# Performance work log

Measured on AMD Instinct MI355X. Metric: run time of the kernel, lower is better.

The kernel has to match this reference:

```python
import jax, jax.numpy as jnp
import numpy as np
from jax import lax

B, C, H, W = 8, 256, 64, 64
A = 9                      # anchors per location (3 scales x 3 ratios)
STRIDE = 16
IMG = 1024                 # image_size
POST_NMS = 1000            # post_nms_top_n (also used as pre-NMS slice, as in source)
NMS_THR = 0.7
BBOX_XFORM_CLIP = 4.135166556742356  # log(1000/16)


def make_anchors():
    # ordering must match torch reshape (B,4,-1): index = a*H*W + h*W + w
    scales = jnp.array([128.0, 256.0, 512.0], dtype=jnp.float32)
    ratios = jnp.array([0.5, 1.0, 2.0], dtype=jnp.float32)
    ws = (scales[:, None] / jnp.sqrt(ratios)[None, :]).reshape(-1)  # [A]
    hs = (scales[:, None] * jnp.sqrt(ratios)[None, :]).reshape(-1)  # [A]
    cx = (jnp.arange(W, dtype=jnp.float32) + 0.5) * STRIDE
    cy = (jnp.arange(H, dtype=jnp.float32) + 0.5) * STRIDE
    cx = jnp.broadcast_to(cx[None, None, :], (A, H, W))
    cy = jnp.broadcast_to(cy[None, :, None], (A, H, W))
    aw = jnp.broadcast_to(ws[:, None, None], (A, H, W))
    ah = jnp.broadcast_to(hs[:, None, None], (A, H, W))
    anchors = jnp.stack([cx - aw / 2, cy - ah / 2, cx + aw / 2, cy + ah / 2], axis=-1)
    return anchors.reshape(-1, 4)  # [K,4] xyxy


def conv2d(x, w, b, pad):
    y = lax.conv_general_dilated(x, w, (1, 1), [(pad, pad), (pad, pad)],
                                 dimension_numbers=("NCHW", "OIHW", "NCHW"))
    return y + b[None, :, None, None]


def decode(t, anchors):
    # t: [K,4] (tx,ty,tw,th); anchors: [K,4] xyxy -> boxes xyxy
    aw = anchors[:, 2] - anchors[:, 0]
    ah = anchors[:, 3] - anchors[:, 1]
    acx = anchors[:, 0] + 0.5 * aw
    acy = anchors[:, 1] + 0.5 * ah
    cx = t[:, 0] * aw + acx
    cy = t[:, 1] * ah + acy
    w = jnp.exp(jnp.clip(t[:, 2], -BBOX_XFORM_CLIP, BBOX_XFORM_CLIP)) * aw
    h = jnp.exp(jnp.clip(t[:, 3], -BBOX_XFORM_CLIP, BBOX_XFORM_CLIP)) * ah
    return jnp.stack([cx - 0.5 * w, cy - 0.5 * h, cx + 0.5 * w, cy + 0.5 * h], axis=-1)


def box_iou(a, b):
    area_a = (a[:, 2] - a[:, 0]) * (a[:, 3] - a[:, 1])
    area_b = (b[:, 2] - b[:, 0]) * (b[:, 3] - b[:, 1])
    lt = jnp.maximum(a[:, None, :2], b[None, :, :2])
    rb = jnp.minimum(a[:, None, 2:], b[None, :, 2:])
    wh = jnp.clip(rb - lt, 0.0)
    inter = wh[..., 0] * wh[..., 1]
    return inter / (area_a[:, None] + area_b[None, :] - inter)


def filter_one(boxes, scores):
    # boxes [K,4], scores [K]. Faithful to source: torch.sort ascending,
    # slice to POST_NMS, then class-agnostic greedy NMS, pad to POST_NMS.
    order = jnp.argsort(lax.stop_gradient(scores))        # ascending (torch.sort default)
    idx = order[:POST_NMS]
    b = boxes[idx]
    s = scores[idx]
    # batched_nms internally processes boxes in descending-score order
    o2 = jnp.argsort(-lax.stop_gradient(s))
    b2 = b[o2]
    s2 = s[o2]
    iou = box_iou(b2, b2)  # [POST_NMS, POST_NMS]
    N = POST_NMS
    pos = jnp.arange(N)

    def body(i, keep):
        sup = (iou[i] > NMS_THR) & (pos > i) & keep[i]
        return keep & ~sup

    keep = lax.fori_loop(0, N, body, jnp.ones((N,), dtype=bool))
    # pack kept boxes (descending-score order) to the front, zero-pad the rest
    perm = jnp.argsort(jnp.where(keep, pos, N + pos))
    valid = pos < jnp.sum(keep)
    out_b = jnp.where(valid[:, None], b2[perm], 0.0)
    out_s = jnp.where(valid, s2[perm], 0.0)
    return out_b, out_s


def setup_inputs() -> dict:
    key = jax.random.key(0)
    ks = jax.random.split(key, 5)
    x = jax.random.normal(ks[0], (B, C, H, W), dtype=jnp.float32)
    conv_w = jax.random.normal(ks[1], (C, C, 3, 3), dtype=jnp.float32) * 0.01
    conv_b = jnp.zeros((C,), dtype=jnp.float32)
    box_w = jax.random.normal(ks[2], (4 * A, C, 1, 1), dtype=jnp.float32) * 0.01
    box_b = jnp.zeros((4 * A,), dtype=jnp.float32)
    obj_w = jax.random.normal(ks[3], (A, C, 1, 1), dtype=jnp.float32) * 0.01
    obj_b = jnp.zeros((A,), dtype=jnp.float32)
    return {"x": x, "conv_w": conv_w, "conv_b": conv_b,
            "box_w": box_w, "box_b": box_b, "obj_w": obj_w, "obj_b": obj_b}


def reference(x, conv_w, conv_b, box_w, box_b, obj_w, obj_b):
    feats = jax.nn.relu(conv2d(x, conv_w, conv_b, 1))        # [B,C,H,W]
    t = conv2d(feats, box_w, box_b, 0)                        # [B,4A,H,W]
    o = conv2d(feats, obj_w, obj_b, 0)                        # [B,A,H,W]
    t = t.reshape(B, 4, -1).transpose(0, 2, 1)                # [B,K,4]
    obj = o.reshape(B, -1)                                    # [B,K]
    anchors = make_anchors()                                  # [K,4]
    props = jax.vmap(lambda ti: decode(ti, anchors))(t)       # [B,K,4]
    props = jnp.clip(props, 0.0, float(IMG))                  # clip_boxes_to_image
    out_b, out_s = jax.vmap(filter_one)(props, obj)           # [B,POST_NMS,4],[B,POST_NMS]
    return jnp.concatenate([out_b, out_s[..., None]], axis=-1)  # [B,POST_NMS,5]
```

## Files before the change

### kernel.cpp

```cpp
#include <hip/hip_runtime.h>

#define B_ 8
#define C_ 256
#define H_ 64
#define W_ 64
#define HW_ 4096
#define HP_ 66
#define HWP_ 4224
#define A_ 9
#define SITES 36864
#define NPOST 1000
#define XCLIPF 4.1351666f
#define IMGF 1024.0f

__device__ inline unsigned keyf(float v) {
  unsigned u = __float_as_uint(v);
  return (u & 0x80000000u) ? ~u : (u | 0x80000000u);
}

__device__ __forceinline__ float dpp_shr1(float v) {
  return __int_as_float(__builtin_amdgcn_update_dpp(
      0, __float_as_int(v), 0x111 , 0xf, 0xf, true));
}
__device__ __forceinline__ float dpp_shl1(float v) {
  return __int_as_float(__builtin_amdgcn_update_dpp(
      0, __float_as_int(v), 0x101 , 0xf, 0xf, true));
}

__global__ __launch_bounds__(256) void pad_x(
    const float* __restrict__ x, float* __restrict__ xp) {
  int t = blockIdx.x * 256 + threadIdx.x;
  int c4 = t & 15;
  int rr = (t >> 4) % HP_;
  int bc = t / (HP_ * 16);
  float4 v = make_float4(0.f, 0.f, 0.f, 0.f);
  if (rr >= 1 && rr <= 64)
    v = ((const float4*)x)[(size_t)bc * (HW_ / 4) + (size_t)(rr - 1) * 16 + c4];
  ((float4*)xp)[(size_t)bc * (HWP_ / 4) + (size_t)rr * 16 + c4] = v;
}

__global__ __launch_bounds__(256, 2) void conv3_4co(
    const float* __restrict__ xp, const float* __restrict__ w,
    const float* __restrict__ bias, float* __restrict__ feats) {
#pragma clang fp contract(off)
  int b       = blockIdx.x & 7;
  int j       = blockIdx.x >> 3;
  int quad    = j & 63;
  int quarter = j >> 6;
  int co0 = quad << 2;
  int row16 = threadIdx.x >> 4;
  int chunk = threadIdx.x & 15;
  int gr = (quarter << 4) + row16;
  int c0 = chunk << 2;

  const float* px0 = xp + (size_t)b * C_ * HWP_ + (size_t)gr * W_ + c0;
  const float* wp0 = w + (size_t)(co0 + 0) * (C_ * 9);
  const float* wp1 = w + (size_t)(co0 + 1) * (C_ * 9);
  const float* wp2 = w + (size_t)(co0 + 2) * (C_ * 9);
  const float* wp3 = w + (size_t)(co0 + 3) * (C_ * 9);

  float acc[4][4][9];
#pragma unroll
  for (int q = 0; q < 4; ++q)
#pragma unroll
    for (int p = 0; p < 4; ++p)
#pragma unroll
      for (int t = 0; t < 9; ++t) acc[q][p][t] = 0.f;

#pragma unroll 2
  for (int ci = 0; ci < C_; ++ci) {
    const float* pr = px0 + (size_t)ci * HWP_;
    float4 tA = ((const float4*)(pr      ))[0];
    float4 mA = ((const float4*)(pr +  64))[0];
    float4 bA = ((const float4*)(pr + 128))[0];

    float T[6], M[6], Bo[6];
    T[1]=tA.x;  T[2]=tA.y;  T[3]=tA.z;  T[4]=tA.w;
    M[1]=mA.x;  M[2]=mA.y;  M[3]=mA.z;  M[4]=mA.w;
    Bo[1]=bA.x; Bo[2]=bA.y; Bo[3]=bA.z; Bo[4]=bA.w;

    T[0]  = dpp_shr1(T[4]);   T[5]  = dpp_shl1(T[1]);
    M[0]  = dpp_shr1(M[4]);   M[5]  = dpp_shl1(M[1]);
    Bo[0] = dpp_shr1(Bo[4]);  Bo[5] = dpp_shl1(Bo[1]);

    float w9[4][9];
#pragma unroll
    for (int t = 0; t < 9; ++t) w9[0][t] = wp0[ci * 9 + t];
#pragma unroll
    for (int t = 0; t < 9; ++t) w9[1][t] = wp1[ci * 9 + t];
#pragma unroll
    for (int t = 0; t < 9; ++t) w9[2][t] = wp2[ci * 9 + t];
#pragma unroll
    for (int t = 0; t < 9; ++t) w9[3][t] = wp3[ci * 9 + t];

#pragma unroll
    for (int q = 0; q < 4; ++q)
#pragma unroll
      for (int p = 0; p < 4; ++p) {
        acc[q][p][0] = fmaf(w9[q][0], T[p],     acc[q][p][0]);
        acc[q][p][1] = fmaf(w9[q][1], T[p+1],   acc[q][p][1]);
        acc[q][p][2] = fmaf(w9[q][2], T[p+2],   acc[q][p][2]);
        acc[q][p][3] = fmaf(w9[q][3], M[p],     acc[q][p][3]);
        acc[q][p][4] = fmaf(w9[q][4], M[p+1],   acc[q][p][4]);
        acc[q][p][5] = fmaf(w9[q][5], M[p+2],   acc[q][p][5]);
        acc[q][p][6] = fmaf(w9[q][6], Bo[p],    acc[q][p][6]);
        acc[q][p][7] = fmaf(w9[q][7], Bo[p+1],  acc[q][p][7]);
        acc[q][p][8] = fmaf(w9[q][8], Bo[p+2],  acc[q][p][8]);
      }
  }

#pragma unroll
  for (int q = 0; q < 4; ++q) {
    float bv = bias[co0 + q];
    float ov[4];
#pragma unroll
    for (int p = 0; p < 4; ++p) {
      float a = 0.f;
#pragma unroll
      for (int t = 0; t < 9; ++t) a = a + acc[q][p][t];
      a = a + bv;
      ov[p] = a > 0.f ? a : 0.f;
    }
    float4* fo = (float4*)(feats + ((size_t)b * C_ + co0 + q) * HW_ + (size_t)gr * W_ + c0);
    fo[0] = make_float4(ov[0], ov[1], ov[2], ov[3]);
  }
}

__global__ __launch_bounds__(256) void conv1_split3(
    const float* __restrict__ feats,
    const float* __restrict__ box_w, const float* __restrict__ box_b,
    const float* __restrict__ obj_w, const float* __restrict__ obj_b,
    float* __restrict__ tbox, float* __restrict__ scores) {
#pragma clang fp contract(off)
  int gidx = blockIdx.x * 256 + threadIdx.x;
  int cgrp = gidx >> 15;
  int rem  = gidx & 32767;
  int b  = rem >> 12;
  int hw = rem & 4095;
  int cbase = cgrp * 15;
  const float* f = feats + (size_t)b * C_ * HW_ + hw;
  const float* wrow[15];
#pragma unroll
  for (int jj = 0; jj < 15; ++jj) {
    int c = cbase + jj;
    wrow[jj] = (c < 36) ? (box_w + (size_t)c * C_) : (obj_w + (size_t)(c - 36) * C_);
  }
  float acc[15];
#pragma unroll
  for (int jj = 0; jj < 15; ++jj) acc[jj] = 0.f;
  for (int ci = 0; ci < C_; ++ci) {
    float fv = f[(size_t)ci * HW_];
#pragma unroll
    for (int jj = 0; jj < 15; ++jj)
      acc[jj] = fmaf(wrow[jj][ci], fv, acc[jj]);
  }
#pragma unroll
  for (int jj = 0; jj < 15; ++jj) {
    int c = cbase + jj;
    if (c < 36) {
      int k = c / 9, a = c - k * 9;
      tbox[(size_t)b * 4 * SITES + (size_t)k * SITES + (size_t)a * HW_ + hw] = acc[jj] + box_b[c];
    } else {
      int a = c - 36;
      scores[(size_t)b * SITES + (size_t)a * HW_ + hw] = acc[jj] + obj_b[a];
    }
  }
}

__global__ __launch_bounds__(1024) void radix_select(
    const float* __restrict__ scores, unsigned* __restrict__ Kout,
    int* __restrict__ needEq, int* __restrict__ cnt, int* __restrict__ eqCnt) {
  int b = blockIdx.x;
  const float* s = scores + (size_t)b * SITES;
  __shared__ unsigned hist[256];
  __shared__ unsigned sh_prefix, sh_mask, sh_cless;
  __shared__ int sh_target;
  if (threadIdx.x == 0) { sh_prefix = 0; sh_mask = 0; sh_target = NPOST - 1; sh_cless = 0; }
  for (int shift = 24; shift >= 0; shift -= 8) {
    if (threadIdx.x < 256) hist[threadIdx.x] = 0;
    __syncthreads();
    unsigned prefix = sh_prefix, mask = sh_mask;
    for (int i = threadIdx.x; i < SITES; i += 1024) {
      unsigned k = keyf(s[i]);
      if ((k & mask) == prefix) atomicAdd(&hist[(k >> shift) & 255u], 1u);
    }
    __syncthreads();
    if (threadIdx.x == 0) {
      unsigned cum = 0; int t = sh_target; int v = 0;
      for (; v < 256; ++v) {
        unsigned h = hist[v];
        if (cum + h > (unsigned)t) break;
        cum += h;
      }
      sh_prefix |= ((unsigned)v) << shift;
      sh_mask   |= 0xFFu << shift;
      sh_target  = t - (int)cum;
      sh_cless  += cum;
    }
    __syncthreads();
  }
  if (threadIdx.x == 0) {
    Kout[b] = sh_prefix;
    needEq[b] = NPOST - (int)sh_cless;
    cnt[b] = 0;
    eqCnt[b] = 0;
  }
}

__global__ __launch_bounds__(256) void compact_sel(
    const float* __restrict__ scores, const unsigned* __restrict__ Kout,
    int* __restrict__ cnt, int* __restrict__ sel,
    int* __restrict__ eqCnt, int* __restrict__ eqList) {
  int b = blockIdx.x / 144;
  int i = (blockIdx.x % 144) * 256 + threadIdx.x;
  unsigned K = Kout[b];
  unsigned k = keyf(scores[(size_t)b * SITES + i]);
  if (k < K) {
    int pos = atomicAdd(&cnt[b], 1);
    sel[b * 1024 + pos] = i;
  } else if (k == K) {
    int e = atomicAdd(&eqCnt[b], 1);
    if (e < 4096) eqList[b * 4096 + e] = i;
  }
}

__global__ __launch_bounds__(256) void fix_eq(
    const int* __restrict__ cnt, const int* __restrict__ needEq,
    const int* __restrict__ eqCnt, const int* __restrict__ eqList,
    int* __restrict__ sel) {
  int b = blockIdx.x;
  int E = eqCnt[b]; if (E > 4096) E = 4096;
  int need = needEq[b];
  int base = cnt[b];
  const int* el = eqList + b * 4096;
  for (int t = threadIdx.x; t < E; t += 256) {
    int site = el[t];
    int rank = 0;
    for (int q = 0; q < E; ++q) rank += (el[q] < site);
    if (rank < need) sel[b * 1024 + base + rank] = site;
  }
}

__global__ __launch_bounds__(128) void order_decode(
    const float* __restrict__ scores, const int* __restrict__ sel,
    const float* __restrict__ tbox, float* __restrict__ s2, float* __restrict__ b2) {
#pragma clang fp contract(off)
  int b   = blockIdx.x >> 3;
  int r   = ((blockIdx.x & 7) * 125) + threadIdx.x;
  __shared__ float ss[NPOST];
  __shared__ int st[NPOST];
  for (int t = threadIdx.x; t < NPOST; t += 128) {
    int site = sel[b * 1024 + t];
    st[t] = site;
    ss[t] = scores[(size_t)b * SITES + site];
  }
  __syncthreads();
  if (threadIdx.x < 125) {
    float sr = ss[r]; int sir = st[r];
    int d = 0;
    for (int q = 0; q < NPOST; ++q) {
      float sq = ss[q];
      d += (int)((sq > sr) || (sq == sr && st[q] < sir));
    }
    s2[(size_t)b * NPOST + d] = sr;
    int site = sir;
    int a = site / HW_;
    int hw = site - a * HW_;
    int h = hw / W_, wc = hw - h * W_;
    int sidx = a / 3, ridx = a - sidx * 3;
    float scale = (sidx == 0) ? 128.f : ((sidx == 1) ? 256.f : 512.f);
    float ratio = (ridx == 0) ? 0.5f : ((ridx == 1) ? 1.0f : 2.0f);
    float sq = sqrtf(ratio);
    float wsa = scale / sq;
    float hsa = scale * sq;
    float cx = ((float)wc + 0.5f) * 16.f;
    float cy = ((float)h + 0.5f) * 16.f;
    float ax1 = cx - wsa * 0.5f;
    float ay1 = cy - hsa * 0.5f;
    float ax2 = cx + wsa * 0.5f;
    float ay2 = cy + hsa * 0.5f;
    float aw = ax2 - ax1, ah = ay2 - ay1;
    float m1 = 0.5f * aw, m2 = 0.5f * ah;
    float acx = ax1 + m1, acy = ay1 + m2;
    const float* tb = tbox + (size_t)b * 4 * SITES + site;
    float t0 = tb[0];
    float t1 = tb[SITES];
    float t2 = tb[2 * (size_t)SITES];
    float t3 = tb[3 * (size_t)SITES];
    if (t2 < -XCLIPF) t2 = -XCLIPF;
    if (t2 > XCLIPF) t2 = XCLIPF;
    if (t3 < -XCLIPF) t3 = -XCLIPF;
    if (t3 > XCLIPF) t3 = XCLIPF;
    float pm0 = t0 * aw;  float pcx = pm0 + acx;
    float pm1 = t1 * ah;  float pcy = pm1 + acy;
    float pw = expf(t2) * aw;
    float ph = expf(t3) * ah;
    float hw0 = 0.5f * pw, hh0 = 0.5f * ph;
    float x1 = pcx - hw0, y1 = pcy - hh0;
    float x2 = pcx + hw0, y2 = pcy + hh0;
    x1 = x1 < 0.f ? 0.f : (x1 > IMGF ? IMGF : x1);
    y1 = y1 < 0.f ? 0.f : (y1 > IMGF ? IMGF : y1);
    x2 = x2 < 0.f ? 0.f : (x2 > IMGF ? IMGF : x2);
    y2 = y2 < 0.f ? 0.f : (y2 > IMGF ? IMGF : y2);
    float* o = b2 + ((size_t)b * NPOST + d) * 4;
    o[0] = x1; o[1] = y1; o[2] = x2; o[3] = y2;
  }
}

__global__ __launch_bounds__(256) void mask_kernel(
    const float* __restrict__ b2, unsigned long long* __restrict__ sup) {
#pragma clang fp contract(off)
  int b = blockIdx.x / 63;
  int i0 = (blockIdx.x % 63) * 16;
  __shared__ float bs[NPOST * 4];
  __shared__ float area[NPOST];
  for (int t = threadIdx.x; t < NPOST * 4; t += 256) bs[t] = b2[(size_t)b * NPOST * 4 + t];
  __syncthreads();
  for (int t = threadIdx.x; t < NPOST; t += 256)
    area[t] = (bs[t * 4 + 2] - bs[t * 4]) * (bs[t * 4 + 3] - bs[t * 4 + 1]);
  __syncthreads();
  int i = i0 + (threadIdx.x & 15);
  int wd = threadIdx.x >> 4;
  if (i >= NPOST) return;
  float ax1 = bs[i * 4], ay1 = bs[i * 4 + 1], ax2 = bs[i * 4 + 2], ay2 = bs[i * 4 + 3];
  float aa = area[i];
  unsigned long long m = 0;
  for (int bit = 0; bit < 64; ++bit) {
    int j = wd * 64 + bit;
    if (j > i && j < NPOST) {
      float lx = fmaxf(ax1, bs[j * 4]);
      float ly = fmaxf(ay1, bs[j * 4 + 1]);
      float rx = fminf(ax2, bs[j * 4 + 2]);
      float ry = fminf(ay2, bs[j * 4 + 3]);
      float iw = rx - lx; if (iw < 0.f) iw = 0.f;
      float ih = ry - ly; if (ih < 0.f) ih = 0.f;
      float inter = iw * ih;
      float denom = (aa + area[j]) - inter;
      float iou = inter / denom;
      if (iou > 0.7f) m |= 1ull << bit;
    }
  }
  sup[((size_t)b * NPOST + i) * 16 + wd] = m;
}

__global__ __launch_bounds__(64) void nms_out(
    const unsigned long long* __restrict__ sup, const float* __restrict__ b2,
    const float* __restrict__ s2, float* __restrict__ out) {
  int b = blockIdx.x;
  int lane = threadIdx.x;
  unsigned long long kw = 0;
  if (lane < 16) kw = (lane < 15) ? ~0ull : ((1ull << 40) - 1);
  const unsigned long long* ms = sup + (size_t)b * NPOST * 16;
  unsigned long long mb[8];
#pragma unroll
  for (int k = 0; k < 8; ++k)
    mb[k] = (lane < 16) ? ms[(size_t)k * 16 + lane] : 0ull;
  for (int i0 = 0; i0 < NPOST; i0 += 8) {
    unsigned long long nb[8];
#pragma unroll
    for (int k = 0; k < 8; ++k) {
      int nx = i0 + 8 + k;
      nb[k] = (nx < NPOST && lane < 16) ? ms[(size_t)nx * 16 + lane] : 0ull;
    }
#pragma unroll
    for (int k = 0; k < 8; ++k) {
      int i = i0 + k;
      unsigned long long w = __shfl(kw, i >> 6, 64);
      if ((w >> (i & 63)) & 1ull) {
        if (lane < 16) kw &= ~mb[k];
      }
    }
#pragma unroll
    for (int k = 0; k < 8; ++k) mb[k] = nb[k];
  }
  __shared__ unsigned long long keeps[16];
  if (lane < 16) keeps[lane] = kw;
  __syncthreads();
  int total = 0;
#pragma unroll
  for (int k = 0; k < 16; ++k) total += __popcll(keeps[k]);
  for (int i = lane; i < NPOST; i += 64) {
    int w = i >> 6;
    int before = 0;
    for (int k = 0; k < w; ++k) before += __popcll(keeps[k]);
    before += __popcll(keeps[w] & ((1ull << (i & 63)) - 1));
    bool kept = (keeps[w] >> (i & 63)) & 1ull;
    if (kept) {
      size_t ob = (size_t)b * (NPOST * 5) + (size_t)before * 5;
      const float* src = b2 + ((size_t)b * NPOST + i) * 4;
      out[ob + 0] = src[0];
      out[ob + 1] = src[1];
      out[ob + 2] = src[2];
      out[ob + 3] = src[3];
      out[ob + 4] = s2[(size_t)b * NPOST + i];
    }
    if (i >= total) {
      size_t ob = (size_t)b * (NPOST * 5) + (size_t)i * 5;
      for (int c = 0; c < 5; ++c) out[ob + c] = 0.f;
    }
  }
}

extern "C" void kernel_launch(void* const* d_in, const int* in_sizes, int n_in,
                              void* d_out, int out_size, void* d_ws, size_t ws_size,
                              hipStream_t stream) {
  const float *x = nullptr, *conv_w = nullptr, *conv_b = nullptr,
              *box_w = nullptr, *box_b = nullptr, *obj_w = nullptr, *obj_b = nullptr;
  for (int i = 0; i < n_in; ++i) {
    switch (in_sizes[i]) {
      case 8388608: x = (const float*)d_in[i]; break;
      case 589824:  conv_w = (const float*)d_in[i]; break;
      case 256:     conv_b = (const float*)d_in[i]; break;
      case 9216:    box_w = (const float*)d_in[i]; break;
      case 36:      box_b = (const float*)d_in[i]; break;
      case 2304:    obj_w = (const float*)d_in[i]; break;
      case 9:       obj_b = (const float*)d_in[i]; break;
    }
  }
  float* out = (float*)d_out;

  char* p = (char*)d_ws;
  auto alloc = [&](size_t n) { char* q = p; p += (n + 255) & ~255ull; return (void*)q; };
  float* feats  = (float*)alloc((size_t)B_ * C_ * HW_ * 4);
  float* tbox   = (float*)alloc((size_t)B_ * 4 * SITES * 4);
  float* scores = (float*)alloc((size_t)B_ * SITES * 4);
  float* xpad   = (float*)alloc((size_t)B_ * C_ * HWP_ * 4);
  unsigned* Kout = (unsigned*)alloc(B_ * 4);
  int* needEq    = (int*)alloc(B_ * 4);
  int* cnt       = (int*)alloc(B_ * 4);
  int* eqCnt     = (int*)alloc(B_ * 4);
  int* eqList    = (int*)alloc((size_t)B_ * 4096 * 4);
  int* sel       = (int*)alloc((size_t)B_ * 1024 * 4);
  float* s2      = (float*)alloc((size_t)B_ * NPOST * 4);
  float* b2      = (float*)alloc((size_t)B_ * NPOST * 4 * 4);
  unsigned long long* sup = (unsigned long long*)alloc((size_t)B_ * NPOST * 16 * 8);

  hipLaunchKernelGGL(pad_x, dim3(B_ * C_ * HP_ * 16 / 256), dim3(256), 0, stream, x, xpad);
  hipLaunchKernelGGL(conv3_4co, dim3(B_ * 64 * 4), dim3(256), 0, stream,
                     xpad, conv_w, conv_b, feats);
  hipLaunchKernelGGL(conv1_split3, dim3(3 * B_ * HW_ / 256), dim3(256), 0, stream,
                     feats, box_w, box_b, obj_w, obj_b, tbox, scores);
  hipLaunchKernelGGL(radix_select, dim3(B_), dim3(1024), 0, stream,
                     scores, Kout, needEq, cnt, eqCnt);
  hipLaunchKernelGGL(compact_sel, dim3(B_ * 144), dim3(256), 0, stream,
                     scores, Kout, cnt, sel, eqCnt, eqList);
  hipLaunchKernelGGL(fix_eq, dim3(B_), dim3(256), 0, stream,
                     cnt, needEq, eqCnt, eqList, sel);
  hipLaunchKernelGGL(order_decode, dim3(B_ * 8), dim3(128), 0, stream,
                     scores, sel, tbox, s2, b2);
  hipLaunchKernelGGL(mask_kernel, dim3(B_ * 63), dim3(256), 0, stream, b2, sup);
  hipLaunchKernelGGL(nms_out, dim3(B_), dim3(64), 0, stream, sup, b2, s2, out);
}
```

Before: 1.020 ms.

## Fuse top-k select, compaction, tie fix and sort-decode into one kernel; pack conv weights

Merges radix_select, compact_sel, fix_eq and order_decode into a single per-batch 1024-thread kernel that keeps the selection lists in shared memory, removing three launches and global round-trips. It also adds a pack_w kernel that reorders conv weights so the four output channels' 36 weights per input channel are contiguous, for more uniform scalar loads in the 3x3 conv. The fused kernel runs only 8 blocks and does the compaction serially per block instead of over 1152 blocks, which lowers parallelism. Weight packing runs on every call, adding a small kernel.

Result: faster. 978.9 us (-4.0%).

```diff
diff --git a/kernel.cpp b/kernel.cpp
--- a/kernel.cpp
+++ b/kernel.cpp
@@ -39,8 +39,19 @@
   ((float4*)xp)[(size_t)bc * (HWP_ / 4) + (size_t)rr * 16 + c4] = v;
 }
 
+__global__ __launch_bounds__(256) void pack_w(
+    const float* __restrict__ w, float* __restrict__ wq) {
+  int idx = blockIdx.x * 256 + threadIdx.x;
+  int quad = idx / (256 * 36);
+  int rem  = idx % (256 * 36);
+  int ci = rem / 36;
+  int k  = rem % 36;
+  int q = k / 9, t = k % 9;
+  wq[idx] = w[((size_t)(quad * 4 + q)) * (C_ * 9) + (size_t)ci * 9 + t];
+}
+
 __global__ __launch_bounds__(256, 2) void conv3_4co(
-    const float* __restrict__ xp, const float* __restrict__ w,
+    const float* __restrict__ xp, const float* __restrict__ wq,
     const float* __restrict__ bias, float* __restrict__ feats) {
 #pragma clang fp contract(off)
   int b       = blockIdx.x & 7;
@@ -54,10 +65,7 @@
   int c0 = chunk << 2;
 
   const float* px0 = xp + (size_t)b * C_ * HWP_ + (size_t)gr * W_ + c0;
-  const float* wp0 = w + (size_t)(co0 + 0) * (C_ * 9);
-  const float* wp1 = w + (size_t)(co0 + 1) * (C_ * 9);
-  const float* wp2 = w + (size_t)(co0 + 2) * (C_ * 9);
-  const float* wp3 = w + (size_t)(co0 + 3) * (C_ * 9);
+  const float* wqb = wq + (size_t)quad * (C_ * 36);
 
   float acc[4][4][9];
 #pragma unroll
@@ -83,15 +91,12 @@
     M[0]  = dpp_shr1(M[4]);   M[5]  = dpp_shl1(M[1]);
     Bo[0] = dpp_shr1(Bo[4]);  Bo[5] = dpp_shl1(Bo[1]);
 
+    const float* wrow = wqb + ci * 36;
     float w9[4][9];
 #pragma unroll
-    for (int t = 0; t < 9; ++t) w9[0][t] = wp0[ci * 9 + t];
-#pragma unroll
-    for (int t = 0; t < 9; ++t) w9[1][t] = wp1[ci * 9 + t];
-#pragma unroll
-    for (int t = 0; t < 9; ++t) w9[2][t] = wp2[ci * 9 + t];
-#pragma unroll
-    for (int t = 0; t < 9; ++t) w9[3][t] = wp3[ci * 9 + t];
+    for (int q = 0; q < 4; ++q)
+#pragma unroll
+      for (int t = 0; t < 9; ++t) w9[q][t] = wrow[q * 9 + t];
 
 #pragma unroll
     for (int q = 0; q < 4; ++q)
@@ -167,15 +172,24 @@
   }
 }
 
-__global__ __launch_bounds__(1024) void radix_select(
-    const float* __restrict__ scores, unsigned* __restrict__ Kout,
-    int* __restrict__ needEq, int* __restrict__ cnt, int* __restrict__ eqCnt) {
+__global__ __launch_bounds__(1024) void select_sort_decode(
+    const float* __restrict__ scores, const float* __restrict__ tbox,
+    float* __restrict__ s2, float* __restrict__ b2) {
+#pragma clang fp contract(off)
   int b = blockIdx.x;
   const float* s = scores + (size_t)b * SITES;
   __shared__ unsigned hist[256];
   __shared__ unsigned sh_prefix, sh_mask, sh_cless;
   __shared__ int sh_target;
-  if (threadIdx.x == 0) { sh_prefix = 0; sh_mask = 0; sh_target = NPOST - 1; sh_cless = 0; }
+  __shared__ int sh_cnt, sh_eq;
+  __shared__ int sh_sel[1024];
+  __shared__ int sh_eqList[4096];
+  __shared__ float ss[NPOST];
+  __shared__ int st[NPOST];
+  if (threadIdx.x == 0) {
+    sh_prefix = 0; sh_mask = 0; sh_target = NPOST - 1; sh_cless = 0;
+    sh_cnt = 0; sh_eq = 0;
+  }
   for (int shift = 24; shift >= 0; shift -= 8) {
     if (threadIdx.x < 256) hist[threadIdx.x] = 0;
     __syncthreads();
@@ -199,63 +213,38 @@
     }
     __syncthreads();
   }
-  if (threadIdx.x == 0) {
-    Kout[b] = sh_prefix;
-    needEq[b] = NPOST - (int)sh_cless;
-    cnt[b] = 0;
-    eqCnt[b] = 0;
-  }
-}
-
-__global__ __launch_bounds__(256) void compact_sel(
-    const float* __restrict__ scores, const unsigned* __restrict__ Kout,
-    int* __restrict__ cnt, int* __restrict__ sel,
-    int* __restrict__ eqCnt, int* __restrict__ eqList) {
-  int b = blockIdx.x / 144;
-  int i = (blockIdx.x % 144) * 256 + threadIdx.x;
-  unsigned K = Kout[b];
-  unsigned k = keyf(scores[(size_t)b * SITES + i]);
-  if (k < K) {
-    int pos = atomicAdd(&cnt[b], 1);
-    sel[b * 1024 + pos] = i;
-  } else if (k == K) {
-    int e = atomicAdd(&eqCnt[b], 1);
-    if (e < 4096) eqList[b * 4096 + e] = i;
-  }
-}
-
-__global__ __launch_bounds__(256) void fix_eq(
-    const int* __restrict__ cnt, const int* __restrict__ needEq,
-    const int* __restrict__ eqCnt, const int* __restrict__ eqList,
-    int* __restrict__ sel) {
-  int b = blockIdx.x;
-  int E = eqCnt[b]; if (E > 4096) E = 4096;
-  int need = needEq[b];
-  int base = cnt[b];
-  const int* el = eqList + b * 4096;
-  for (int t = threadIdx.x; t < E; t += 256) {
-    int site = el[t];
-    int rank = 0;
-    for (int q = 0; q < E; ++q) rank += (el[q] < site);
-    if (rank < need) sel[b * 1024 + base + rank] = site;
-  }
-}
-
-__global__ __launch_bounds__(128) void order_decode(
-    const float* __restrict__ scores, const int* __restrict__ sel,
-    const float* __restrict__ tbox, float* __restrict__ s2, float* __restrict__ b2) {
-#pragma clang fp contract(off)
-  int b   = blockIdx.x >> 3;
-  int r   = ((blockIdx.x & 7) * 125) + threadIdx.x;
-  __shared__ float ss[NPOST];
-  __shared__ int st[NPOST];
-  for (int t = threadIdx.x; t < NPOST; t += 128) {
-    int site = sel[b * 1024 + t];
+  unsigned K = sh_prefix;
+  int need = NPOST - (int)sh_cless;
+  for (int i = threadIdx.x; i < SITES; i += 1024) {
+    unsigned k = keyf(s[i]);
+    if (k < K) {
+      int pos = atomicAdd(&sh_cnt, 1);
+      sh_sel[pos] = i;
+    } else if (k == K) {
+      int e = atomicAdd(&sh_eq, 1);
+      if (e < 4096) sh_eqList[e] = i;
+    }
+  }
+  __syncthreads();
+  {
+    int E = sh_eq; if (E > 4096) E = 4096;
+    int base = sh_cnt;
+    for (int t = threadIdx.x; t < E; t += 1024) {
+      int site = sh_eqList[t];
+      int rank = 0;
+      for (int q = 0; q < E; ++q) rank += (sh_eqList[q] < site);
+      if (rank < need) sh_sel[base + rank] = site;
+    }
+  }
+  __syncthreads();
+  for (int t = threadIdx.x; t < NPOST; t += 1024) {
+    int site = sh_sel[t];
     st[t] = site;
-    ss[t] = scores[(size_t)b * SITES + site];
-  }
-  __syncthreads();
-  if (threadIdx.x < 125) {
+    ss[t] = s[site];
+  }
+  __syncthreads();
+  if (threadIdx.x < NPOST) {
+    int r = threadIdx.x;
     float sr = ss[r]; int sir = st[r];
     int d = 0;
     for (int q = 0; q < NPOST; ++q) {
@@ -425,29 +414,19 @@
   float* tbox   = (float*)alloc((size_t)B_ * 4 * SITES * 4);
   float* scores = (float*)alloc((size_t)B_ * SITES * 4);
   float* xpad   = (float*)alloc((size_t)B_ * C_ * HWP_ * 4);
-  unsigned* Kout = (unsigned*)alloc(B_ * 4);
-  int* needEq    = (int*)alloc(B_ * 4);
-  int* cnt       = (int*)alloc(B_ * 4);
-  int* eqCnt     = (int*)alloc(B_ * 4);
-  int* eqList    = (int*)alloc((size_t)B_ * 4096 * 4);
-  int* sel       = (int*)alloc((size_t)B_ * 1024 * 4);
-  float* s2      = (float*)alloc((size_t)B_ * NPOST * 4);
-  float* b2      = (float*)alloc((size_t)B_ * NPOST * 4 * 4);
+  float* wq     = (float*)alloc((size_t)64 * C_ * 36 * 4);
+  float* s2     = (float*)alloc((size_t)B_ * NPOST * 4);
+  float* b2     = (float*)alloc((size_t)B_ * NPOST * 4 * 4);
   unsigned long long* sup = (unsigned long long*)alloc((size_t)B_ * NPOST * 16 * 8);
 
   hipLaunchKernelGGL(pad_x, dim3(B_ * C_ * HP_ * 16 / 256), dim3(256), 0, stream, x, xpad);
+  hipLaunchKernelGGL(pack_w, dim3(64 * C_ * 36 / 256), dim3(256), 0, stream, conv_w, wq);
   hipLaunchKernelGGL(conv3_4co, dim3(B_ * 64 * 4), dim3(256), 0, stream,
-                     xpad, conv_w, conv_b, feats);
+                     xpad, wq, conv_b, feats);
   hipLaunchKernelGGL(conv1_split3, dim3(3 * B_ * HW_ / 256), dim3(256), 0, stream,
                      feats, box_w, box_b, obj_w, obj_b, tbox, scores);
-  hipLaunchKernelGGL(radix_select, dim3(B_), dim3(1024), 0, stream,
-                     scores, Kout, needEq, cnt, eqCnt);
-  hipLaunchKernelGGL(compact_sel, dim3(B_ * 144), dim3(256), 0, stream,
-                     scores, Kout, cnt, sel, eqCnt, eqList);
-  hipLaunchKernelGGL(fix_eq, dim3(B_), dim3(256), 0, stream,
-                     cnt, needEq, eqCnt, eqList, sel);
-  hipLaunchKernelGGL(order_decode, dim3(B_ * 8), dim3(128), 0, stream,
-                     scores, sel, tbox, s2, b2);
+  hipLaunchKernelGGL(select_sort_decode, dim3(B_), dim3(1024), 0, stream,
+                     scores, tbox, s2, b2);
   hipLaunchKernelGGL(mask_kernel, dim3(B_ * 63), dim3(256), 0, stream, b2, sup);
   hipLaunchKernelGGL(nms_out, dim3(B_), dim3(64), 0, stream, sup, b2, s2, out);
 }
```
